# Kernel optimization log

Measured on AMD Instinct MI355X. Metric: run time of the kernel, lower is better.

The kernel has to match this reference:

```python
import jax, jax.numpy as jnp
import numpy as np
from jax import lax

C = 128      # channels
H = 128
W = 128
B = 2
WS = 4       # window size
HEADS = 4
HID = int(C * 2.66)  # 340
EPS = 1e-6


def conv1x1(x, w):
    # x: [b,c,h,w], w: [out,in]
    return jnp.einsum('oc,bchw->bohw', w, x)


def dwconv3(x, w):
    # depthwise 3x3, w: [c,1,3,3]
    return lax.conv_general_dilated(
        x, w, window_strides=(1, 1), padding='SAME',
        feature_group_count=x.shape[1],
        dimension_numbers=('NCHW', 'OIHW', 'NCHW'))


def layernorm(x, w, b):
    # channel-wise LN over dim 1 (per pixel), w/b: [C]
    m = x.mean(axis=1, keepdims=True)
    v = ((x - m) ** 2).mean(axis=1, keepdims=True)
    xn = (x - m) / jnp.sqrt(v + EPS)
    return xn * w[None, :, None, None] + b[None, :, None, None]


def l2norm(x):
    n = jnp.sqrt(jnp.sum(x * x, axis=-1, keepdims=True))
    return x / jnp.maximum(n, 1e-12)


def rsa(x, qkv_w, dw_w, proj_w, temp):
    b, c, h, w = x.shape
    ws = WS
    x_ = jnp.roll(x, (-ws // 2, -ws // 2), axis=(2, 3))  # shifts > 0
    qkv = dwconv3(conv1x1(x_, qkv_w), dw_w)
    q, k, v = jnp.split(qkv, 3, axis=1)

    def win(t):  # b c (h dh) (w dw) -> b (h w) (dh dw) c
        return t.reshape(b, c, h // ws, ws, w // ws, ws) \
                .transpose(0, 2, 4, 3, 5, 1) \
                .reshape(b, (h // ws) * (w // ws), ws * ws, c)

    q, k, v = win(q), win(k), win(v)
    q = l2norm(q)
    k = l2norm(k)
    # attn = q^T @ k  -> [b, nw, c, c]
    attn = jax.nn.relu(jnp.einsum('bnpc,bnpd->bncd', q, k) * temp[0, 0, 0])
    out = jnp.einsum('bnpc,bncd->bnpd', v, attn)  # v @ attn
    out = out.reshape(b, h // ws, w // ws, ws, ws, c) \
             .transpose(0, 5, 1, 3, 2, 4).reshape(b, c, h, w)
    out = jnp.roll(out, (ws // 2, ws // 2), axis=(2, 3))
    return conv1x1(out, proj_w)


def gsa(x, qkv_w, dw_w, proj_w, temp):
    b, c, h, w = x.shape
    hd = HEADS
    ch = c // hd
    qkv = dwconv3(conv1x1(x, qkv_w), dw_w)
    q, k, v = jnp.split(qkv, 3, axis=1)

    def hs(t):  # b (head c) h w -> b head c (h w)
        return t.reshape(b, hd, ch, h * w)

    q, k, v = hs(q), hs(k), hs(v)
    q = l2norm(q)
    k = l2norm(k)
    attn = jax.nn.relu(jnp.einsum('bhcn,bhdn->bhcd', q, k) * temp[0, 0, 0])
    out = jnp.einsum('bhcd,bhdn->bhcn', attn, v).reshape(b, c, h, w)
    return conv1x1(out, proj_w)


def ffn(x, w_in, w_dw, w_out):
    h = dwconv3(conv1x1(x, w_in), w_dw)
    h = jax.nn.gelu(h, approximate=False)
    return conv1x1(h, w_out)


def setup_inputs() -> dict:
    key = jax.random.key(0)
    ks = jax.random.split(key, 16)
    s = 0.05
    d = {
        'x': jax.random.normal(ks[0], (B, C, H, W), jnp.float32),
        # spatial (RSA) branch
        'w_s0': jnp.ones((C,), jnp.float32), 'b_s0': jnp.zeros((C,), jnp.float32),
        'w_s2': jnp.ones((C,), jnp.float32), 'b_s2': jnp.zeros((C,), jnp.float32),
        'rsa_qkv': jax.random.normal(ks[1], (3 * C, C), jnp.float32) * s,
        'rsa_dw': jax.random.normal(ks[2], (3 * C, 1, 3, 3), jnp.float32) * s,
        'rsa_proj': jax.random.normal(ks[3], (C, C), jnp.float32) * s,
        'rsa_temp': jnp.ones((1, 1, 1), jnp.float32),
        'ffs_in': jax.random.normal(ks[4], (HID, C), jnp.float32) * s,
        'ffs_dw': jax.random.normal(ks[5], (HID, 1, 3, 3), jnp.float32) * s,
        'ffs_out': jax.random.normal(ks[6], (C, HID), jnp.float32) * s,
        # channel (GSA) branch
        'w_c0': jnp.ones((C,), jnp.float32), 'b_c0': jnp.zeros((C,), jnp.float32),
        'w_c2': jnp.ones((C,), jnp.float32), 'b_c2': jnp.zeros((C,), jnp.float32),
        'gsa_qkv': jax.random.normal(ks[7], (3 * C, C), jnp.float32) * s,
        'gsa_dw': jax.random.normal(ks[8], (3 * C, 1, 3, 3), jnp.float32) * s,
        'gsa_proj': jax.random.normal(ks[9], (C, C), jnp.float32) * s,
        'gsa_temp': jnp.ones((1, 1, 1), jnp.float32),
        'ffc_in': jax.random.normal(ks[10], (HID, C), jnp.float32) * s,
        'ffc_dw': jax.random.normal(ks[11], (HID, 1, 3, 3), jnp.float32) * s,
        'ffc_out': jax.random.normal(ks[12], (C, HID), jnp.float32) * s,
    }
    return d


def reference(x, w_s0, b_s0, w_s2, b_s2, rsa_qkv, rsa_dw, rsa_proj, rsa_temp,
              ffs_in, ffs_dw, ffs_out,
              w_c0, b_c0, w_c2, b_c2, gsa_qkv, gsa_dw, gsa_proj, gsa_temp,
              ffc_in, ffc_dw, ffc_out):
    # shared_depth = 1: only the i==0 branches execute
    # spatial block (RSA)
    x_ = rsa(layernorm(x, w_s0, b_s0), rsa_qkv, rsa_dw, rsa_proj, rsa_temp)
    x = ffn(layernorm(x_ + x, w_s2, b_s2), ffs_in, ffs_dw, ffs_out) + x_
    # channel block (GSA)
    x_ = gsa(layernorm(x, w_c0, b_c0), gsa_qkv, gsa_dw, gsa_proj, gsa_temp)
    x = ffn(layernorm(x_ + x, w_c2, b_c2), ffc_in, ffc_dw, ffc_out) + x_
    return x
```

## Files before the change

kernel.cpp:

```cpp
#include <hip/hip_runtime.h>
#include <hip/hip_bf16.h>
#include <math.h>

typedef __hip_bfloat16 bf16;
typedef __attribute__((ext_vector_type(8))) short short8;
typedef __attribute__((ext_vector_type(4))) short short4v;
typedef __attribute__((ext_vector_type(4))) float float4v;

static constexpr int cB  = 2;
static constexpr int cC  = 128;
static constexpr int cH  = 128;
static constexpr int cW  = 128;
static constexpr int cP  = cH * cW;
static constexpr int cC3 = 384;
static constexpr int cHID = 340;
static constexpr int cNW = 1024;
static constexpr float cEPS = 1e-6f;

__device__ __forceinline__ float bfu2f(unsigned short u){
  union { unsigned int i; float f; } c; c.i = ((unsigned int)u) << 16; return c.f;
}
__device__ __forceinline__ unsigned short f2b(float f){
  union { float f; unsigned int u; } c; c.f = f;
  unsigned int r = c.u + 0x7FFFu + ((c.u >> 16) & 1u);
  return (unsigned short)(r >> 16);
}

__global__ void k_wcvt(const float* __restrict__ qkv_s, const float* __restrict__ qkv_c,
                       const float* __restrict__ fin_s, const float* __restrict__ fin_c,
                       const float* __restrict__ prj_s, const float* __restrict__ prj_c,
                       const float* __restrict__ fo_s,  const float* __restrict__ fo_c,
                       unsigned short* __restrict__ WB, float* __restrict__ S){
  int i = blockIdx.x * 256 + threadIdx.x;
  if (i >= 319488){
    int j = i - 319488;
    if (j < 8704) S[j] = 0.f;
    return;
  }
  float v;
  if (i < 98304){
    v = (i < 49152) ? qkv_s[i] : qkv_c[i - 49152];
  } else if (i < 196608){
    int j = (i < 147456) ? (i - 98304) : (i - 147456);
    int row = j >> 7, col = j & 127;
    const float* src = (i < 147456) ? fin_s : fin_c;
    v = (row < cHID) ? src[row * 128 + col] : 0.f;
  } else if (i < 229376){
    v = (i < 212992) ? prj_s[i - 196608] : prj_c[i - 212992];
  } else {
    int j = (i < 274432) ? (i - 229376) : (i - 274432);
    int row = j / 352, col = j - row * 352;
    const float* src = (i < 274432) ? fo_s : fo_c;
    v = (col < cHID) ? src[row * cHID + col] : 0.f;
  }
  WB[i] = f2b(v);
}

__global__ void __launch_bounds__(256) k_ln(const float* __restrict__ a,
                                            const float* __restrict__ gamma,
                                            const float* __restrict__ beta,
                                            unsigned short* __restrict__ out, int sh, int sw){
  int idx = blockIdx.x * 256 + threadIdx.x;
  if (idx >= cB * cP) return;
  int b = idx >> 14;
  int p = idx & (cP - 1);
  const float* ap = a + (size_t)b * cC * cP + p;
  float s = 0.f, ss = 0.f;
  #pragma unroll 8
  for (int c = 0; c < cC; c++){
    float v = ap[c * cP];
    s += v; ss += v * v;
  }
  float m = s * (1.f / cC);
  float var = ss * (1.f / cC) - m * m;
  float rstd = rsqrtf(var + cEPS);
  int h = p >> 7, w = p & 127;
  int h2 = (h + sh) & (cH - 1);
  int w2 = (w + sw) & (cW - 1);
  unsigned short* op = out + (size_t)b * cP * cC + (size_t)(h2 * cW + w2) * cC;
  #pragma unroll
  for (int c8 = 0; c8 < cC; c8 += 8){
    short8 tv;
    #pragma unroll
    for (int j = 0; j < 8; j++){
      float v = ap[(c8 + j) * cP];
      tv[j] = (short)f2b((v - m) * rstd * gamma[c8 + j] + beta[c8 + j]);
    }
    *(short8*)(op + c8) = tv;
  }
}

__global__ void __launch_bounds__(256) k_gemm(const unsigned short* __restrict__ Wb,
                                              const unsigned short* __restrict__ Xg,
                                              unsigned short* __restrict__ Out,
                                              int K, int PK, int PM){
  __shared__ short Wls[128 * 40];
  __shared__ short Xls[64 * 40];
  int b  = blockIdx.z;
  int p0 = blockIdx.x * 64;
  int m0 = blockIdx.y * 128;
  int t  = threadIdx.x;
  int lanelo = t & 15;
  int quad   = (t >> 4) & 3;
  int wv = t >> 6;
  int w1 = wv & 1;
  int w2 = wv >> 1;
  int srw = t >> 1;
  int kow = (t & 1) * 16;
  int srx = t >> 2;
  int kox = (t & 3) * 8;

  float4v acc[2][4];
  #pragma unroll
  for (int i = 0; i < 2; i++)
    #pragma unroll
    for (int j = 0; j < 4; j++)
      acc[i][j] = (float4v){0.f, 0.f, 0.f, 0.f};

  const unsigned short* Xb = Xg + (size_t)b * cP * PK;

  for (int k0 = 0; k0 < K; k0 += 32){
    short8 xv  = *(const short8*)(Xb + (size_t)(p0 + srx) * PK + k0 + kox);
    short8 wv0 = *(const short8*)(Wb + (size_t)(m0 + srw) * K + k0 + kow);
    short8 wv1 = *(const short8*)(Wb + (size_t)(m0 + srw) * K + k0 + kow + 8);
    __syncthreads();
    *(short8*)&Wls[srw * 40 + kow]     = wv0;
    *(short8*)&Wls[srw * 40 + kow + 8] = wv1;
    *(short8*)&Xls[srx * 40 + kox]     = xv;
    __syncthreads();
    short8 af[2], bfr[4];
    #pragma unroll
    for (int i = 0; i < 2; i++)
      af[i] = *(const short8*)&Xls[(w1 * 32 + i * 16 + lanelo) * 40 + quad * 8];
    #pragma unroll
    for (int j = 0; j < 4; j++)
      bfr[j] = *(const short8*)&Wls[(w2 * 64 + j * 16 + lanelo) * 40 + quad * 8];
    #pragma unroll
    for (int i = 0; i < 2; i++)
      #pragma unroll
      for (int j = 0; j < 4; j++)
        acc[i][j] = __builtin_amdgcn_mfma_f32_16x16x32_bf16(af[i], bfr[j], acc[i][j], 0, 0, 0);
  }
  unsigned short* Ob = Out + (size_t)b * cP * PM;
  #pragma unroll
  for (int i = 0; i < 2; i++)
    #pragma unroll
    for (int j = 0; j < 4; j++){
      int wrow = m0 + w2 * 64 + j * 16 + lanelo;
      if (wrow >= PM) continue;
      #pragma unroll
      for (int r = 0; r < 4; r++){
        int pix = p0 + w1 * 32 + i * 16 + quad * 4 + r;
        Ob[(size_t)pix * PM + wrow] = f2b(acc[i][j][r]);
      }
    }
}

template<int MODE>
__global__ void __launch_bounds__(256) k_gemm64(const unsigned short* __restrict__ Wb,
                                                const unsigned short* __restrict__ Xg,
                                                const float* __restrict__ R,
                                                const float* __restrict__ Base,
                                                const float* __restrict__ gamma,
                                                const float* __restrict__ beta,
                                                float* __restrict__ Tr,
                                                unsigned short* __restrict__ LNo,
                                                int K, int PK){
  __shared__ short SMEM[8704];
  __shared__ float gls[128], bls[128];
  __shared__ float psum[64], pssq[64];
  short* Wls = SMEM;
  short* Xls = SMEM + 5120;
  int b  = blockIdx.z;
  int p0 = blockIdx.x * 64;
  int t  = threadIdx.x;
  int lanelo = t & 15;
  int quad   = (t >> 4) & 3;
  int wv = t >> 6;
  int w2 = wv >> 1, w1 = wv & 1;
  int srw = t >> 1;
  int kow = (t & 1) * 16;
  int srx = t >> 2;
  int kox = (t & 3) * 8;

  if (MODE != 3){
    if (t < 128){ gls[t] = gamma[t]; bls[t] = beta[t]; }
    if (t < 64){ psum[t] = 0.f; pssq[t] = 0.f; }
  }

  float4v acc[4][2];
  #pragma unroll
  for (int i = 0; i < 4; i++){
    acc[i][0] = (float4v){0.f, 0.f, 0.f, 0.f};
    acc[i][1] = (float4v){0.f, 0.f, 0.f, 0.f};
  }
  const unsigned short* Xb = Xg + (size_t)b * cP * PK;

  for (int k0 = 0; k0 < K; k0 += 32){
    short8 xv = *(const short8*)(Xb + (size_t)(p0 + srx) * PK + k0 + kox);
    short8 wv0 = *(const short8*)(Wb + (size_t)srw * K + k0 + kow);
    short8 wv1 = *(const short8*)(Wb + (size_t)srw * K + k0 + kow + 8);
    __syncthreads();
    *(short8*)&Wls[srw * 40 + kow]     = wv0;
    *(short8*)&Wls[srw * 40 + kow + 8] = wv1;
    *(short8*)&Xls[srx * 40 + kox]     = xv;
    __syncthreads();
    short8 af[4], bfr[2];
    #pragma unroll
    for (int i = 0; i < 4; i++)
      af[i] = *(const short8*)&Wls[(w2 * 64 + i * 16 + lanelo) * 40 + quad * 8];
    #pragma unroll
    for (int j = 0; j < 2; j++)
      bfr[j] = *(const short8*)&Xls[(w1 * 32 + j * 16 + lanelo) * 40 + quad * 8];
    #pragma unroll
    for (int i = 0; i < 4; i++)
      #pragma unroll
      for (int j = 0; j < 2; j++)
        acc[i][j] = __builtin_amdgcn_mfma_f32_16x16x32_bf16(af[i], bfr[j], acc[i][j], 0, 0, 0);
  }
  float lnv[4][2][4];
  #pragma unroll
  for (int i = 0; i < 4; i++)
    #pragma unroll
    for (int j = 0; j < 2; j++){
      int n = p0 + w1 * 32 + j * 16 + lanelo;
      #pragma unroll
      for (int r = 0; r < 4; r++){
        int m = w2 * 64 + i * 16 + quad * 4 + r;
        size_t idx = (size_t)b * cC * cP + (size_t)m * cP + n;
        float v = acc[i][j][r];
        if (MODE >= 2) v += R[idx];
        Tr[idx] = v;
        if (MODE == 1) v += Base[idx];
        lnv[i][j][r] = v;
      }
    }
  if (MODE == 3) return;
  __syncthreads();
  #pragma unroll
  for (int j = 0; j < 2; j++){
    int nl = w1 * 32 + j * 16 + lanelo;
    float s = 0.f, ss = 0.f;
    #pragma unroll
    for (int i = 0; i < 4; i++)
      #pragma unroll
      for (int r = 0; r < 4; r++){
        float v = lnv[i][j][r];
        s += v; ss += v * v;
      }
    atomicAdd(&psum[nl], s);
    atomicAdd(&pssq[nl], ss);
  }
  __syncthreads();
  #pragma unroll
  for (int j = 0; j < 2; j++){
    int nl = w1 * 32 + j * 16 + lanelo;
    float mean = psum[nl] * (1.f / cC);
    float var = pssq[nl] * (1.f / cC) - mean * mean;
    float rstd = rsqrtf(var + cEPS);
    #pragma unroll
    for (int i = 0; i < 4; i++)
      #pragma unroll
      for (int r = 0; r < 4; r++){
        int m = w2 * 64 + i * 16 + quad * 4 + r;
        SMEM[nl * 136 + m] = (short)f2b((lnv[i][j][r] - mean) * rstd * gls[m] + bls[m]);
      }
  }
  __syncthreads();
  unsigned short* Ob = LNo + (size_t)b * cP * cC;
  #pragma unroll
  for (int rr = 0; rr < 4; rr++){
    int id = t + rr * 256;
    int row = id >> 4, col8 = (id & 15) * 8;
    short8 sv = *(const short8*)&SMEM[row * 136 + col8];
    *(short8*)(Ob + (size_t)(p0 + row) * cC + col8) = sv;
  }
}

template<int GELU, int CCn, int PITCH>
__global__ void __launch_bounds__(256) k_dw(const unsigned short* __restrict__ in,
                                            const float* __restrict__ wt,
                                            unsigned short* __restrict__ out){
  __shared__ float wls[16 * 76];
  int t = threadIdx.x;
  int cbase = blockIdx.y * 128;
  for (int i = t; i < 16 * 72; i += 256){
    int cg = i / 72, rem = i - cg * 72;
    int tap = rem >> 3, j = rem & 7;
    int c = cbase + cg * 8 + j;
    wls[cg * 76 + rem] = (c < CCn) ? wt[c * 9 + tap] : 0.f;
  }
  __syncthreads();
  int cgl = t & 15, pixl = t >> 4;
  int c0 = cbase + cgl * 8;
  if (c0 >= PITCH) return;
  int p = blockIdx.x * 16 + pixl;
  int h = p >> 7, w = p & 127;
  int b = blockIdx.z;
  const unsigned short* ib = in + (size_t)b * cP * PITCH;
  float4 wreg[18];
  #pragma unroll
  for (int q = 0; q < 18; q++)
    wreg[q] = *(const float4*)&wls[cgl * 76 + q * 4];
  short8 v[9];
  #pragma unroll
  for (int ky = 0; ky < 3; ky++){
    int hh = h + ky - 1;
    bool okh = (unsigned)hh < (unsigned)cH;
    int hc = okh ? hh : h;
    #pragma unroll
    for (int kx = 0; kx < 3; kx++){
      int ww = w + kx - 1;
      bool okw = (unsigned)ww < (unsigned)cW;
      int wc = okw ? ww : w;
      short8 lv = *(const short8*)(ib + (size_t)(hc * cW + wc) * PITCH + c0);
      if (!(okh && okw)) lv = (short8){0,0,0,0,0,0,0,0};
      v[ky * 3 + kx] = lv;
    }
  }
  float acc[8] = {0,0,0,0,0,0,0,0};
  #pragma unroll
  for (int tap = 0; tap < 9; tap++){
    float4 w0 = wreg[tap * 2];
    float4 w1 = wreg[tap * 2 + 1];
    float wa[8] = {w0.x, w0.y, w0.z, w0.w, w1.x, w1.y, w1.z, w1.w};
    #pragma unroll
    for (int j = 0; j < 8; j++)
      acc[j] += wa[j] * bfu2f((unsigned short)v[tap][j]);
  }
  short8 ov;
  #pragma unroll
  for (int j = 0; j < 8; j++){
    float vv = acc[j];
    if (GELU) vv = 0.5f * vv * (1.f + erff(vv * 0.70710678118654752f));
    ov[j] = (short)f2b(vv);
  }
  *(short8*)(out + (size_t)b * cP * PITCH + (size_t)p * PITCH + c0) = ov;
}

__global__ void __launch_bounds__(256) k_rsa(const unsigned short* __restrict__ qkv,
                                             const float* __restrict__ temp,
                                             unsigned short* __restrict__ out){
  constexpr int QT = 0;
  constexpr int KT = 5120;
  constexpr int VO = 10240;
  constexpr int AT = 12416;
  __shared__ short lds[21632];
  __shared__ float nq[16], nk[16];
  int blk = blockIdx.x;
  int b  = blk >> 10;
  int nw = blk & 1023;
  int hb = nw >> 5, wb = nw & 31;
  int t = threadIdx.x;
  #pragma unroll
  for (int j = 0; j < 5; j++)
    *(short8*)&lds[t * 40 + j * 8] = (short8){0,0,0,0,0,0,0,0};
  if (t < 16) nq[t] = 0.f;
  else if (t < 32) nk[t - 16] = 0.f;
  __syncthreads();
  const unsigned short* base = qkv + (size_t)b * cP * cC3;
  #pragma unroll
  for (int r = 0; r < 3; r++){
    int i = t + 256 * r;
    int pix = i / 48;
    int cg = i - pix * 48;
    int c0 = cg * 8;
    int gp = (hb * 4 + (pix >> 2)) * cW + wb * 4 + (pix & 3);
    short8 v = *(const short8*)(base + (size_t)gp * cC3 + c0);
    if (c0 < 256){
      float s = 0.f;
      #pragma unroll
      for (int e = 0; e < 8; e++){ float f = bfu2f((unsigned short)v[e]); s += f * f; }
      int off = (c0 < 128) ? (QT + c0 * 40) : (KT + (c0 - 128) * 40);
      #pragma unroll
      for (int e = 0; e < 8; e++) lds[off + e * 40 + pix] = v[e];
      atomicAdd((c0 < 128) ? &nq[pix] : &nk[pix], s);
    } else {
      *(short8*)&lds[VO + pix * 136 + (c0 - 256)] = v;
    }
  }
  __syncthreads();
  float T = temp[0];
  #pragma unroll
  for (int r = 0; r < 8; r++){
    int idx = t + 256 * r;
    int c = idx >> 4, p = idx & 15;
    float sc = (1.f / fmaxf(sqrtf(nq[p]), 1e-12f)) * (1.f / fmaxf(sqrtf(nk[p]), 1e-12f));
    int a = QT + c * 40 + p;
    lds[a] = (short)f2b(bfu2f((unsigned short)lds[a]) * sc);
  }
  __syncthreads();
  int lanelo = t & 15;
  int quad = (t >> 4) & 3;
  int wv = t >> 6;
  float4v oacc[2];
  oacc[0] = (float4v){0.f,0.f,0.f,0.f};
  oacc[1] = (float4v){0.f,0.f,0.f,0.f};
  for (int ch = 0; ch < 2; ch++){
    #pragma unroll
    for (int ct = 0; ct < 4; ct++){
      int c0 = ch * 64 + ct * 16;
      short8 af = *(const short8*)&lds[QT + (c0 + lanelo) * 40 + quad * 8];
      #pragma unroll
      for (int dt = 0; dt < 2; dt++){
        int d0 = wv * 32 + dt * 16;
        short8 bf = *(const short8*)&lds[KT + (d0 + lanelo) * 40 + quad * 8];
        float4v acc = __builtin_amdgcn_mfma_f32_16x16x32_bf16(af, bf,
                        (float4v){0.f,0.f,0.f,0.f}, 0, 0, 0);
        short4v sv;
        #pragma unroll
        for (int r2 = 0; r2 < 4; r2++) sv[r2] = (short)f2b(fmaxf(acc[r2] * T, 0.f));
        *(short4v*)&lds[AT + (d0 + lanelo) * 72 + ct * 16 + quad * 4] = sv;
      }
    }
    __syncthreads();
    #pragma unroll
    for (int dt = 0; dt < 2; dt++){
      int d0 = wv * 32 + dt * 16;
      #pragma unroll
      for (int kk = 0; kk < 2; kk++){
        short8 av8 = *(const short8*)&lds[VO + lanelo * 136 + ch * 64 + kk * 32 + quad * 8];
        short8 bv8 = *(const short8*)&lds[AT + (d0 + lanelo) * 72 + kk * 32 + quad * 8];
        oacc[dt] = __builtin_amdgcn_mfma_f32_16x16x32_bf16(av8, bv8, oacc[dt], 0, 0, 0);
      }
    }
    __syncthreads();
  }
  #pragma unroll
  for (int dt = 0; dt < 2; dt++){
    int d = wv * 32 + dt * 16 + lanelo;
    #pragma unroll
    for (int r2 = 0; r2 < 4; r2++){
      int p = quad * 4 + r2;
      int h2 = (hb * 4 + (p >> 2) + 2) & (cH - 1);
      int w2 = (wb * 4 + (p & 3) + 2) & (cW - 1);
      out[(size_t)b * cP * cC + (size_t)(h2 * cW + w2) * cC + d] = f2b(oacc[dt][r2]);
    }
  }
}

__global__ void __launch_bounds__(256) k_gram(const unsigned short* __restrict__ qkv,
                                              float* __restrict__ S,
                                              float* __restrict__ Qn,
                                              float* __restrict__ Kn){
  __shared__ float qs[32][132];
  __shared__ float ks[32][132];
  int blk = blockIdx.x;
  int chunk = blk & 127;
  int bh = blk >> 7;
  int b = bh >> 2, hd = bh & 3;
  int n0 = chunk * 128;
  int t = threadIdx.x;
  {
    int row = t >> 1;
    int half = t & 1;
    const unsigned short* pq = qkv + (size_t)b * cP * cC3 + (size_t)(n0 + row) * cC3 + hd * 32 + half * 16;
    const unsigned short* pk = pq + 128;
    short8 q0 = *(const short8*)pq;
    short8 q1 = *(const short8*)(pq + 8);
    short8 k0 = *(const short8*)pk;
    short8 k1 = *(const short8*)(pk + 8);
    #pragma unroll
    for (int e = 0; e < 8; e++){
      qs[half * 16 + e][row]     = bfu2f((unsigned short)q0[e]);
      qs[half * 16 + 8 + e][row] = bfu2f((unsigned short)q1[e]);
      ks[half * 16 + e][row]     = bfu2f((unsigned short)k0[e]);
      ks[half * 16 + 8 + e][row] = bfu2f((unsigned short)k1[e]);
    }
  }
  __syncthreads();
  if (t < 64){
    const float* row = (t < 32) ? qs[t] : ks[t - 32];
    float s = 0.f;
    #pragma unroll
    for (int i = 0; i < 128; i += 4){
      float4 v = *(const float4*)(row + i);
      s += v.x*v.x + v.y*v.y + v.z*v.z + v.w*v.w;
    }
    if (t < 32) atomicAdd(&Qn[bh * 32 + t], s);
    else        atomicAdd(&Kn[bh * 32 + (t - 32)], s);
  }
  int cc = (t >> 4) * 2;
  int dd = t & 15;
  float a00 = 0.f, a01 = 0.f, a10 = 0.f, a11 = 0.f;
  for (int n = 0; n < 128; n += 4){
    float4 q0 = *(const float4*)&qs[cc][n];
    float4 q1 = *(const float4*)&qs[cc + 1][n];
    float4 k0 = *(const float4*)&ks[dd][n];
    float4 k1 = *(const float4*)&ks[dd + 16][n];
    a00 += q0.x*k0.x + q0.y*k0.y + q0.z*k0.z + q0.w*k0.w;
    a01 += q0.x*k1.x + q0.y*k1.y + q0.z*k1.z + q0.w*k1.w;
    a10 += q1.x*k0.x + q1.y*k0.y + q1.z*k0.z + q1.w*k0.w;
    a11 += q1.x*k1.x + q1.y*k1.y + q1.z*k1.z + q1.w*k1.w;
  }
  float* Sb = S + (size_t)bh * 1024;
  atomicAdd(&Sb[cc * 32 + dd], a00);
  atomicAdd(&Sb[cc * 32 + dd + 16], a01);
  atomicAdd(&Sb[(cc + 1) * 32 + dd], a10);
  atomicAdd(&Sb[(cc + 1) * 32 + dd + 16], a11);
}

__global__ void __launch_bounds__(256) k_apply(const unsigned short* __restrict__ qkv,
                                               const float* __restrict__ S,
                                               const float* __restrict__ Qn,
                                               const float* __restrict__ Kn,
                                               const float* __restrict__ temp,
                                               unsigned short* __restrict__ out){
  __shared__ float at[1024];
  int blk = blockIdx.x;
  int tile = blk & 63;
  int bh = blk >> 6;
  int b = bh >> 2, hd = bh & 3;
  int t = threadIdx.x;
  float T = temp[0];
  for (int i = t; i < 1024; i += 256){
    int c = i >> 5, d = i & 31;
    float nqv = fmaxf(sqrtf(Qn[bh * 32 + c]), 1e-12f);
    float nkv = fmaxf(sqrtf(Kn[bh * 32 + d]), 1e-12f);
    at[i] = fmaxf(S[bh * 1024 + i] / (nqv * nkv) * T, 0.f);
  }
  __syncthreads();
  int n = tile * 256 + t;
  const unsigned short* vb = qkv + (size_t)b * cP * cC3 + (size_t)n * cC3 + 256 + hd * 32;
  float vr[32];
  #pragma unroll
  for (int d8 = 0; d8 < 32; d8 += 8){
    short8 v = *(const short8*)(vb + d8);
    #pragma unroll
    for (int e = 0; e < 8; e++) vr[d8 + e] = bfu2f((unsigned short)v[e]);
  }
  unsigned short* ob = out + (size_t)b * cP * cC + (size_t)n * cC + hd * 32;
  #pragma unroll
  for (int c8 = 0; c8 < 32; c8 += 8){
    short8 ov;
    #pragma unroll
    for (int e = 0; e < 8; e++){
      const float* ar = &at[(c8 + e) * 32];
      float acc = 0.f;
      #pragma unroll
      for (int d = 0; d < 32; d += 4){
        float4 a4 = *(const float4*)(ar + d);
        acc += a4.x * vr[d] + a4.y * vr[d+1] + a4.z * vr[d+2] + a4.w * vr[d+3];
      }
      ov[e] = (short)f2b(acc);
    }
    *(short8*)(ob + c8) = ov;
  }
}

extern "C" void kernel_launch(void* const* d_in, const int* in_sizes, int n_in,
                              void* d_out, int out_size, void* d_ws, size_t ws_size,
                              hipStream_t stream){
  const float* x     = (const float*)d_in[0];
  const float* w_s0  = (const float*)d_in[1];
  const float* b_s0  = (const float*)d_in[2];
  const float* w_s2  = (const float*)d_in[3];
  const float* b_s2  = (const float*)d_in[4];
  const float* rsa_qkv  = (const float*)d_in[5];
  const float* rsa_dw   = (const float*)d_in[6];
  const float* rsa_proj = (const float*)d_in[7];
  const float* rsa_temp = (const float*)d_in[8];
  const float* ffs_in   = (const float*)d_in[9];
  const float* ffs_dw   = (const float*)d_in[10];
  const float* ffs_out  = (const float*)d_in[11];
  const float* w_c0  = (const float*)d_in[12];
  const float* b_c0  = (const float*)d_in[13];
  const float* w_c2  = (const float*)d_in[14];
  const float* b_c2  = (const float*)d_in[15];
  const float* gsa_qkv  = (const float*)d_in[16];
  const float* gsa_dw   = (const float*)d_in[17];
  const float* gsa_proj = (const float*)d_in[18];
  const float* gsa_temp = (const float*)d_in[19];
  const float* ffc_in   = (const float*)d_in[20];
  const float* ffc_dw   = (const float*)d_in[21];
  const float* ffc_out  = (const float*)d_in[22];

  const size_t szC  = (size_t)cB * cC * cP;
  const size_t szC3 = (size_t)cB * cC3 * cP;
  float* XF = (float*)d_ws;
  float* XS = XF + szC;
  unsigned short* LO   = (unsigned short*)(XS + szC);
  unsigned short* Abuf = LO + szC;
  unsigned short* Bbuf = Abuf + szC3;
  float* S  = (float*)(Bbuf + szC3);
  float* Qn = S + 8192;
  float* Kn = Qn + 256;
  float* AT = Kn + 256;
  unsigned short* WB = (unsigned short*)(AT + 1024);
  unsigned short* W_QKV_S = WB;
  unsigned short* W_QKV_C = WB + 49152;
  unsigned short* W_FIN_S = WB + 98304;
  unsigned short* W_FIN_C = WB + 147456;
  unsigned short* W_PRJ_S = WB + 196608;
  unsigned short* W_PRJ_C = WB + 212992;
  unsigned short* W_FO_S  = WB + 229376;
  unsigned short* W_FO_C  = WB + 274432;

  dim3 t256(256);
  dim3 gLN(cB * cP / 256);
  dim3 gG3(cP / 64, 3, cB);
  dim3 gG64(cP / 64, 1, cB);
  dim3 gDW(cP / 16, 3, cB);

  k_wcvt<<<dim3(1282), t256, 0, stream>>>(rsa_qkv, gsa_qkv, ffs_in, ffc_in,
                                          rsa_proj, gsa_proj, ffs_out, ffc_out, WB, S);

  k_ln<<<gLN, t256, 0, stream>>>(x, w_s0, b_s0, LO, 126, 126);
  k_gemm<<<gG3, t256, 0, stream>>>(W_QKV_S, LO, Abuf, 128, 128, 384);
  k_dw<0,384,384><<<gDW, t256, 0, stream>>>(Abuf, rsa_dw, Bbuf);
  k_rsa<<<dim3(cB * cNW), t256, 0, stream>>>(Bbuf, rsa_temp, LO);
  k_gemm64<1><<<gG64, t256, 0, stream>>>(W_PRJ_S, LO, nullptr, x, w_s2, b_s2, XS, LO, 128, 128);
  k_gemm<<<gG3, t256, 0, stream>>>(W_FIN_S, LO, Abuf, 128, 128, 352);
  k_dw<1,340,352><<<gDW, t256, 0, stream>>>(Abuf, ffs_dw, Bbuf);
  k_gemm64<2><<<gG64, t256, 0, stream>>>(W_FO_S, Bbuf, XS, nullptr, w_c0, b_c0, XF, LO, 352, 352);

  k_gemm<<<gG3, t256, 0, stream>>>(W_QKV_C, LO, Abuf, 128, 128, 384);
  k_dw<0,384,384><<<gDW, t256, 0, stream>>>(Abuf, gsa_dw, Bbuf);
  k_gram<<<dim3(1024), t256, 0, stream>>>(Bbuf, S, Qn, Kn);
  k_apply<<<dim3(512), t256, 0, stream>>>(Bbuf, S, Qn, Kn, gsa_temp, LO);
  k_gemm64<1><<<gG64, t256, 0, stream>>>(W_PRJ_C, LO, nullptr, XF, w_c2, b_c2, XS, LO, 128, 128);
  k_gemm<<<gG3, t256, 0, stream>>>(W_FIN_C, LO, Abuf, 128, 128, 352);
  k_dw<1,340,352><<<gDW, t256, 0, stream>>>(Abuf, ffc_dw, Bbuf);
  k_gemm64<3><<<gG64, t256, 0, stream>>>(W_FO_C, Bbuf, XS, nullptr, nullptr, nullptr,
                                         (float*)d_out, nullptr, 352, 352);
}
```

Measured before the change: 359.5 us.

## Stage GEMM/RSA outputs through LDS for vector stores; MFMA-based GSA apply

The GEMM epilogue and the RSA output now write bf16 results to shared memory first, then store them with coalesced 16-byte writes instead of scattered 2-byte stores. The GEMM grid is flattened with a remapped block index so blocks sharing a pixel tile are scheduled together. The GSA apply kernel is rewritten to use MFMA with bf16 attention weights held in LDS, covering all four heads per block. This adds extra barriers and LDS traffic, and rounding the attention matrix to bf16 loses some precision.

```diff
diff --git a/kernel.cpp b/kernel.cpp
--- a/kernel.cpp
+++ b/kernel.cpp
@@ -94,11 +94,17 @@
                                               const unsigned short* __restrict__ Xg,
                                               unsigned short* __restrict__ Out,
                                               int K, int PK, int PM){
-  __shared__ short Wls[128 * 40];
-  __shared__ short Xls[64 * 40];
-  int b  = blockIdx.z;
-  int p0 = blockIdx.x * 64;
-  int m0 = blockIdx.y * 128;
+  __shared__ short SMEM[8704];
+  short* Wls = SMEM;
+  short* Xls = SMEM + 5120;
+  int bid = blockIdx.x;
+  int s  = (bid & 7) * (1536 >> 3) + (bid >> 3);
+  int mt = s % 3;
+  int r3 = s / 3;
+  int pt = r3 & 255;
+  int b  = r3 >> 8;
+  int p0 = pt * 64;
+  int m0 = mt * 128;
   int t  = threadIdx.x;
   int lanelo = t & 15;
   int quad   = (t >> 4) & 3;
@@ -141,19 +147,27 @@
       for (int j = 0; j < 4; j++)
         acc[i][j] = __builtin_amdgcn_mfma_f32_16x16x32_bf16(af[i], bfr[j], acc[i][j], 0, 0, 0);
   }
+  __syncthreads();
+  #pragma unroll
+  for (int i = 0; i < 2; i++)
+    #pragma unroll
+    for (int j = 0; j < 4; j++){
+      int pixloc = w1 * 32 + i * 16 + quad * 4;
+      int mloc   = w2 * 64 + j * 16 + lanelo;
+      #pragma unroll
+      for (int r = 0; r < 4; r++)
+        SMEM[(pixloc + r) * 136 + mloc] = (short)f2b(acc[i][j][r]);
+    }
+  __syncthreads();
   unsigned short* Ob = Out + (size_t)b * cP * PM;
   #pragma unroll
-  for (int i = 0; i < 2; i++)
-    #pragma unroll
-    for (int j = 0; j < 4; j++){
-      int wrow = m0 + w2 * 64 + j * 16 + lanelo;
-      if (wrow >= PM) continue;
-      #pragma unroll
-      for (int r = 0; r < 4; r++){
-        int pix = p0 + w1 * 32 + i * 16 + quad * 4 + r;
-        Ob[(size_t)pix * PM + wrow] = f2b(acc[i][j][r]);
-      }
-    }
+  for (int rr = 0; rr < 4; rr++){
+    int id = t + rr * 256;
+    int row = id >> 4, col8 = (id & 15) * 8;
+    int wcol = m0 + col8;
+    if (wcol < PM)
+      *(short8*)(Ob + (size_t)(p0 + row) * PM + wcol) = *(const short8*)&SMEM[row * 136 + col8];
+  }
 }
 
 template<int MODE>
@@ -432,10 +446,16 @@
     #pragma unroll
     for (int r2 = 0; r2 < 4; r2++){
       int p = quad * 4 + r2;
-      int h2 = (hb * 4 + (p >> 2) + 2) & (cH - 1);
-      int w2 = (wb * 4 + (p & 3) + 2) & (cW - 1);
-      out[(size_t)b * cP * cC + (size_t)(h2 * cW + w2) * cC + d] = f2b(oacc[dt][r2]);
-    }
+      lds[p * 136 + d] = (short)f2b(oacc[dt][r2]);
+    }
+  }
+  __syncthreads();
+  {
+    int px = t >> 4, cg = (t & 15) * 8;
+    int h2 = (hb * 4 + (px >> 2) + 2) & (cH - 1);
+    int w2 = (wb * 4 + (px & 3) + 2) & (cW - 1);
+    short8 sv = *(const short8*)&lds[px * 136 + cg];
+    *(short8*)(out + (size_t)b * cP * cC + (size_t)(h2 * cW + w2) * cC + cg) = sv;
   }
 }
 
@@ -500,51 +520,54 @@
   atomicAdd(&Sb[(cc + 1) * 32 + dd + 16], a11);
 }
 
-__global__ void __launch_bounds__(256) k_apply(const unsigned short* __restrict__ qkv,
-                                               const float* __restrict__ S,
-                                               const float* __restrict__ Qn,
-                                               const float* __restrict__ Kn,
-                                               const float* __restrict__ temp,
-                                               unsigned short* __restrict__ out){
-  __shared__ float at[1024];
-  int blk = blockIdx.x;
-  int tile = blk & 63;
-  int bh = blk >> 6;
-  int b = bh >> 2, hd = bh & 3;
+__global__ void __launch_bounds__(256) k_applyM(const unsigned short* __restrict__ qkv,
+                                                const float* __restrict__ S,
+                                                const float* __restrict__ Qn,
+                                                const float* __restrict__ Kn,
+                                                const float* __restrict__ temp,
+                                                unsigned short* __restrict__ out){
+  __shared__ short atb[128 * 40];
+  __shared__ short OT[64 * 136];
+  int b = blockIdx.y;
+  int nbase = blockIdx.x * 64;
   int t = threadIdx.x;
   float T = temp[0];
-  for (int i = t; i < 1024; i += 256){
+  #pragma unroll
+  for (int it = 0; it < 16; it++){
+    int i = t + it * 256;
     int c = i >> 5, d = i & 31;
-    float nqv = fmaxf(sqrtf(Qn[bh * 32 + c]), 1e-12f);
+    int hd = c >> 5, cl = c & 31;
+    int bh = b * 4 + hd;
+    float nqv = fmaxf(sqrtf(Qn[bh * 32 + cl]), 1e-12f);
     float nkv = fmaxf(sqrtf(Kn[bh * 32 + d]), 1e-12f);
-    at[i] = fmaxf(S[bh * 1024 + i] / (nqv * nkv) * T, 0.f);
-  }
-  __syncthreads();
-  int n = tile * 256 + t;
-  const unsigned short* vb = qkv + (size_t)b * cP * cC3 + (size_t)n * cC3 + 256 + hd * 32;
-  float vr[32];
-  #pragma unroll
-  for (int d8 = 0; d8 < 32; d8 += 8){
-    short8 v = *(const short8*)(vb + d8);
-    #pragma unroll
-    for (int e = 0; e < 8; e++) vr[d8 + e] = bfu2f((unsigned short)v[e]);
-  }
-  unsigned short* ob = out + (size_t)b * cP * cC + (size_t)n * cC + hd * 32;
-  #pragma unroll
-  for (int c8 = 0; c8 < 32; c8 += 8){
-    short8 ov;
-    #pragma unroll
-    for (int e = 0; e < 8; e++){
-      const float* ar = &at[(c8 + e) * 32];
-      float acc = 0.f;
-      #pragma unroll
-      for (int d = 0; d < 32; d += 4){
-        float4 a4 = *(const float4*)(ar + d);
-        acc += a4.x * vr[d] + a4.y * vr[d+1] + a4.z * vr[d+2] + a4.w * vr[d+3];
-      }
-      ov[e] = (short)f2b(acc);
-    }
-    *(short8*)(ob + c8) = ov;
+    float v = fmaxf(S[(size_t)bh * 1024 + cl * 32 + d] / (nqv * nkv) * T, 0.f);
+    atb[c * 40 + d] = (short)f2b(v);
+  }
+  __syncthreads();
+  int lanelo = t & 15, quad = (t >> 4) & 3, wv = t >> 6;
+  int n0 = nbase + wv * 16;
+  const unsigned short* vb = qkv + (size_t)b * cP * cC3 + (size_t)(n0 + lanelo) * cC3 + 256 + quad * 8;
+  #pragma unroll
+  for (int hd = 0; hd < 4; hd++){
+    short8 af = *(const short8*)(vb + hd * 32);
+    #pragma unroll
+    for (int cth = 0; cth < 2; cth++){
+      int c0 = hd * 32 + cth * 16;
+      short8 bf = *(const short8*)&atb[(c0 + lanelo) * 40 + quad * 8];
+      float4v acc = __builtin_amdgcn_mfma_f32_16x16x32_bf16(af, bf,
+                      (float4v){0.f,0.f,0.f,0.f}, 0, 0, 0);
+      #pragma unroll
+      for (int r = 0; r < 4; r++)
+        OT[(wv * 16 + quad * 4 + r) * 136 + c0 + lanelo] = (short)f2b(acc[r]);
+    }
+  }
+  __syncthreads();
+  unsigned short* ob = out + (size_t)b * cP * cC;
+  #pragma unroll
+  for (int rr = 0; rr < 4; rr++){
+    int id = t + rr * 256;
+    int row = id >> 4, col8 = (id & 15) * 8;
+    *(short8*)(ob + (size_t)(nbase + row) * cC + col8) = *(const short8*)&OT[row * 136 + col8];
   }
 }
 
@@ -598,7 +621,7 @@
 
   dim3 t256(256);
   dim3 gLN(cB * cP / 256);
-  dim3 gG3(cP / 64, 3, cB);
+  dim3 gG1(cP / 64 * 3 * cB);
   dim3 gG64(cP / 64, 1, cB);
   dim3 gDW(cP / 16, 3, cB);
 
@@ -606,20 +629,20 @@
                                           rsa_proj, gsa_proj, ffs_out, ffc_out, WB, S);
 
   k_ln<<<gLN, t256, 0, stream>>>(x, w_s0, b_s0, LO, 126, 126);
-  k_gemm<<<gG3, t256, 0, stream>>>(W_QKV_S, LO, Abuf, 128, 128, 384);
+  k_gemm<<<gG1, t256, 0, stream>>>(W_QKV_S, LO, Abuf, 128, 128, 384);
   k_dw<0,384,384><<<gDW, t256, 0, stream>>>(Abuf, rsa_dw, Bbuf);
   k_rsa<<<dim3(cB * cNW), t256, 0, stream>>>(Bbuf, rsa_temp, LO);
   k_gemm64<1><<<gG64, t256, 0, stream>>>(W_PRJ_S, LO, nullptr, x, w_s2, b_s2, XS, LO, 128, 128);
-  k_gemm<<<gG3, t256, 0, stream>>>(W_FIN_S, LO, Abuf, 128, 128, 352);
+  k_gemm<<<gG1, t256, 0, stream>>>(W_FIN_S, LO, Abuf, 128, 128, 352);
   k_dw<1,340,352><<<gDW, t256, 0, stream>>>(Abuf, ffs_dw, Bbuf);
   k_gemm64<2><<<gG64, t256, 0, stream>>>(W_FO_S, Bbuf, XS, nullptr, w_c0, b_c0, XF, LO, 352, 352);
 
-  k_gemm<<<gG3, t256, 0, stream>>>(W_QKV_C, LO, Abuf, 128, 128, 384);
+  k_gemm<<<gG1, t256, 0, stream>>>(W_QKV_C, LO, Abuf, 128, 128, 384);
   k_dw<0,384,384><<<gDW, t256, 0, stream>>>(Abuf, gsa_dw, Bbuf);
   k_gram<<<dim3(1024), t256, 0, stream>>>(Bbuf, S, Qn, Kn);
-  k_apply<<<dim3(512), t256, 0, stream>>>(Bbuf, S, Qn, Kn, gsa_temp, LO);
+  k_applyM<<<dim3(cP / 64, cB), t256, 0, stream>>>(Bbuf, S, Qn, Kn, gsa_temp, LO);
   k_gemm64<1><<<gG64, t256, 0, stream>>>(W_PRJ_C, LO, nullptr, XF, w_c2, b_c2, XS, LO, 128, 128);
-  k_gemm<<<gG3, t256, 0, stream>>>(W_FIN_C, LO, Abuf, 128, 128, 352);
+  k_gemm<<<gG1, t256, 0, stream>>>(W_FIN_C, LO, Abuf, 128, 128, 352);
   k_dw<1,340,352><<<gDW, t256, 0, stream>>>(Abuf, ffc_dw, Bbuf);
   k_gemm64<3><<<gG64, t256, 0, stream>>>(W_FO_C, Bbuf, XS, nullptr, nullptr, nullptr,
                                          (float*)d_out, nullptr, 352, 352);
```

Result: no change. 365.0 us (+1.5%).
